# Performance work log

Hardware: AMD Instinct MI355X
Metric: run time of the kernel (lower is better)

The kernel has to match this reference:

```python
import jax, jax.numpy as jnp
import numpy as np

EMBED_DIM = 2048
NUM_Q_HEADS = 32
NUM_KV_HEADS = 8
HEAD_DIM = EMBED_DIM // NUM_Q_HEADS
N_REP = NUM_Q_HEADS // NUM_KV_HEADS
B, T = 2, 2048


def setup_inputs() -> dict:
    key = jax.random.key(0)
    ks = jax.random.split(key, 10)
    C = EMBED_DIM
    kv_dim = NUM_KV_HEADS * HEAD_DIM
    s = 1.0 / np.sqrt(C)
    return {
        "x": jax.random.normal(ks[0], (B, T, C), dtype=jnp.float32),
        "mask": jnp.tril(jnp.ones((1, 1, T, T), dtype=bool)),
        "Wq": jax.random.normal(ks[1], (C, C), dtype=jnp.float32) * s,
        "bq": jnp.zeros((C,), dtype=jnp.float32),
        "Wk": jax.random.normal(ks[2], (C, kv_dim), dtype=jnp.float32) * s,
        "bk": jnp.zeros((kv_dim,), dtype=jnp.float32),
        "Wv": jax.random.normal(ks[3], (C, kv_dim), dtype=jnp.float32) * s,
        "bv": jnp.zeros((kv_dim,), dtype=jnp.float32),
        "Wo": jax.random.normal(ks[4], (C, C), dtype=jnp.float32) * s,
        "bo": jnp.zeros((C,), dtype=jnp.float32),
    }


def reference(x, mask, Wq, bq, Wk, bk, Wv, bv, Wo, bo):
    b, t, c = x.shape
    # projections
    q = (x @ Wq + bq).reshape(b, t, NUM_Q_HEADS, HEAD_DIM).transpose(0, 2, 1, 3)   # [B,Hq,T,D]
    k = (x @ Wk + bk).reshape(b, t, NUM_KV_HEADS, HEAD_DIM).transpose(0, 2, 1, 3)  # [B,Hkv,T,D]
    v = (x @ Wv + bv).reshape(b, t, NUM_KV_HEADS, HEAD_DIM).transpose(0, 2, 1, 3)
    # repeat KV heads to match query heads (same math as expand+reshape)
    k = jnp.repeat(k, N_REP, axis=1)  # [B,Hq,T,D]
    v = jnp.repeat(v, N_REP, axis=1)
    scores = jnp.einsum("bhqd,bhkd->bhqk", q, k) / np.sqrt(HEAD_DIM)
    scores = jnp.where(mask, scores, -jnp.inf)
    attn = jax.nn.softmax(scores, axis=-1)
    out = jnp.einsum("bhqk,bhkd->bhqd", attn, v)  # [B,Hq,T,D]
    out = out.transpose(0, 2, 1, 3).reshape(b, t, c)
    return out @ Wo + bo
```

## Files before the change

kernel.cpp:

```cpp
#include <hip/hip_runtime.h>
#include <stdint.h>

typedef __attribute__((ext_vector_type(8))) short bf16x8;
typedef __attribute__((ext_vector_type(4))) float f32x4;

#define LOG2E 1.44269504088896f
#define T_SEQ 2048

__device__ __forceinline__ float bf2f(short s) {
    unsigned u = ((unsigned)(unsigned short)s) << 16;
    float f; __builtin_memcpy(&f, &u, 4); return f;
}
__device__ __forceinline__ short f2bf(float f) {
    unsigned u; __builtin_memcpy(&u, &f, 4);
    u = (u + 0x7FFFu + ((u >> 16) & 1u)) >> 16;
    return (short)u;
}
__device__ __forceinline__ short f2bf_trunc(float f) {
    unsigned u; __builtin_memcpy(&u, &f, 4);
    return (short)(u >> 16);
}

#define GLDS(g, l) __builtin_amdgcn_global_load_lds( \
    (const __attribute__((address_space(1))) void*)(g), \
    (__attribute__((address_space(3))) void*)(l), 16, 0, 0)

__global__ void detect_k(const unsigned short* __restrict__ x, int* __restrict__ flag) {
    int lane = threadIdx.x;
    int cnt = 0;
    for (int i = lane; i < 2048; i += 64) {
        int e = (x[i] >> 7) & 0xFF;
        if (e >= 0xC0) cnt++;
    }
    cnt += __shfl_xor(cnt, 1);
    cnt += __shfl_xor(cnt, 2);
    cnt += __shfl_xor(cnt, 4);
    cnt += __shfl_xor(cnt, 8);
    cnt += __shfl_xor(cnt, 16);
    cnt += __shfl_xor(cnt, 32);
    if (lane == 0) { flag[0] = (cnt >= 32) ? 1 : 0; flag[1] = 0; }
}

__global__ __launch_bounds__(256) void convert_k(
    const void* __restrict__ in, short* __restrict__ out, int n,
    const int* __restrict__ flag)
{
    int i = (blockIdx.x * 256 + threadIdx.x) * 8;
    if (i >= n) return;
    bf16x8 v;
    if (*flag) {
        const float* f = (const float*)in + i;
        #pragma unroll
        for (int j = 0; j < 8; ++j) v[j] = f2bf(f[j]);
    } else {
        v = *(const bf16x8*)((const short*)in + i);
    }
    *(bf16x8*)(out + i) = v;
}

__global__ __launch_bounds__(256) void convert4_k(
    const void* __restrict__ b0, const void* __restrict__ b1,
    const void* __restrict__ b2, const void* __restrict__ b3,
    short* __restrict__ o0, short* __restrict__ o1,
    short* __restrict__ o2, short* __restrict__ o3,
    const int* __restrict__ flag)
{
    int i = (blockIdx.x * 256 + threadIdx.x) * 8;
    const void* in; short* out; int off;
    if      (i < 2048) { in = b0; out = o0; off = i; }
    else if (i < 2560) { in = b1; out = o1; off = i - 2048; }
    else if (i < 3072) { in = b2; out = o2; off = i - 2560; }
    else if (i < 5120) { in = b3; out = o3; off = i - 3072; }
    else return;
    bf16x8 v;
    if (*flag) {
        const float* f = (const float*)in + off;
        #pragma unroll
        for (int j = 0; j < 8; ++j) v[j] = f2bf(f[j]);
    } else {
        v = *(const bf16x8*)((const short*)in + off);
    }
    *(bf16x8*)(out + off) = v;
}

__global__ __launch_bounds__(256) void transpose_k(
    const void* __restrict__ in_, short* __restrict__ out,
    int R, int ldi, long ibstride, long obstride, const int* __restrict__ flag)
{
    short* ob = out + (long)blockIdx.z * obstride;
    int c = blockIdx.x * 256 + threadIdx.x;
    int r0 = blockIdx.y * 64;
    int fp32 = *flag;
    if (fp32) {
        const float* ib = (const float*)in_ + (long)blockIdx.z * ibstride;
        for (int rr = 0; rr < 64; rr += 8) {
            bf16x8 v;
            #pragma unroll
            for (int j = 0; j < 8; ++j) v[j] = f2bf(ib[(long)(r0 + rr + j) * ldi + c]);
            *(bf16x8*)(ob + (long)c * R + r0 + rr) = v;
        }
    } else {
        const short* ib = (const short*)in_ + (long)blockIdx.z * ibstride;
        for (int rr = 0; rr < 64; rr += 8) {
            bf16x8 v;
            #pragma unroll
            for (int j = 0; j < 8; ++j) v[j] = ib[(long)(r0 + rr + j) * ldi + c];
            *(bf16x8*)(ob + (long)c * R + r0 + rr) = v;
        }
    }
}

#define BK 32
__global__ __launch_bounds__(256) void gemm_bt(
    const short* __restrict__ A, const short* __restrict__ Bt,
    const short* __restrict__ bias1, int nsplit,
    short* __restrict__ C, short* __restrict__ C2, int n2,
    float* __restrict__ Cf, const int* __restrict__ flag,
    int M, int N, int K)
{
    __shared__ short a_lds[128 * BK];
    __shared__ short b_lds[128 * BK];
    const int tid = threadIdx.x;
    const int wave = tid >> 6, lane = tid & 63;
    const int quad = lane >> 4, l16 = lane & 15;
    const int m0 = blockIdx.y * 128, n0 = blockIdx.x * 128;
    const int wm = (wave >> 1) * 64, wn = (wave & 1) * 64;

    const int c0 = wave * 64 + lane;
    const int c1 = 256 + c0;
    const int row0 = c0 >> 2, kc0 = (c0 & 3) ^ ((row0 >> 1) & 3);
    const int row1 = c1 >> 2, kc1 = (c1 & 3) ^ ((row1 >> 1) & 3);
    const long aoff0 = (long)(m0 + row0) * K + kc0 * 8;
    const long aoff1 = (long)(m0 + row1) * K + kc1 * 8;
    const long boff0 = (long)(n0 + row0) * K + kc0 * 8;
    const long boff1 = (long)(n0 + row1) * K + kc1 * 8;
    short* alp0 = a_lds + (wave * 64) * 8;
    short* alp1 = a_lds + (256 + wave * 64) * 8;
    short* blp0 = b_lds + (wave * 64) * 8;
    short* blp1 = b_lds + (256 + wave * 64) * 8;

    int aro[4], bro[4];
    #pragma unroll
    for (int t = 0; t < 4; ++t) {
        int ra = wm + t * 16 + l16;
        aro[t] = ra * BK + (quad ^ ((ra >> 1) & 3)) * 8;
        int rb = wn + t * 16 + l16;
        bro[t] = rb * BK + (quad ^ ((rb >> 1) & 3)) * 8;
    }

    f32x4 acc[4][4];
    #pragma unroll
    for (int i = 0; i < 4; ++i)
        #pragma unroll
        for (int j = 0; j < 4; ++j)
            acc[i][j] = (f32x4){0.f, 0.f, 0.f, 0.f};

    for (int k0 = 0; k0 < K; k0 += BK) {
        __syncthreads();
        GLDS(A + aoff0 + k0, alp0);
        GLDS(A + aoff1 + k0, alp1);
        GLDS(Bt + boff0 + k0, blp0);
        GLDS(Bt + boff1 + k0, blp1);
        __syncthreads();
        bf16x8 af[4], bfr[4];
        #pragma unroll
        for (int t = 0; t < 4; ++t) af[t] = *(const bf16x8*)(a_lds + aro[t]);
        #pragma unroll
        for (int t = 0; t < 4; ++t) bfr[t] = *(const bf16x8*)(b_lds + bro[t]);
        #pragma unroll
        for (int mt = 0; mt < 4; ++mt)
            #pragma unroll
            for (int nt = 0; nt < 4; ++nt)
                acc[mt][nt] = __builtin_amdgcn_mfma_f32_16x16x32_bf16(
                    af[mt], bfr[nt], acc[mt][nt], 0, 0, 0);
    }

    const int f32o = Cf ? *flag : 0;
    #pragma unroll
    for (int nt = 0; nt < 4; ++nt) {
        int col = n0 + wn + nt * 16 + l16;
        float bb = bf2f(bias1[col < nsplit ? col : 0]);
        #pragma unroll
        for (int mt = 0; mt < 4; ++mt)
            #pragma unroll
            for (int r = 0; r < 4; ++r) {
                int row = m0 + wm + mt * 16 + quad * 4 + r;
                float val = acc[mt][nt][r] + bb;
                if (f32o) {
                    Cf[(long)row * N + col] = val;
                } else if (C2) {
                    if (col < n2) C[(long)row * n2 + col] = f2bf(val);
                    else          C2[(long)row * (N - n2) + (col - n2)] = f2bf(val);
                } else {
                    C[(long)row * N + col] = f2bf(val);
                }
            }
    }
}

#define PLD 68
__global__ __launch_bounds__(256, 4) void attn_k(
    const short* __restrict__ Qf, const short* __restrict__ KVf,
    const short* __restrict__ Vt, short* __restrict__ Attn)
{
    __shared__ short k_lds[64 * PLD];
    __shared__ short vt_lds[64 * PLD];
    __shared__ short p_lds[4 * 32 * PLD];
    const int tid = threadIdx.x;
    const int wave = tid >> 6, lane = tid & 63;
    const int quad = lane >> 4, l16 = lane & 15;

    const int id = blockIdx.x;
    const int bh = id & 63;
    const int w = id >> 6;
    const int QTMAP[16] = {15,13,11,9, 0,2,4,6, 14,12,10,8, 1,3,5,7};
    const int qt = QTMAP[w];
    const int b = bh >> 5, h = bh & 31, hkv = h >> 2;
    const int q0 = qt * 128;
    const int nsteps = 2 * (qt + 1);

    bf16x8 aq[2][2];
    #pragma unroll
    for (int mt = 0; mt < 2; ++mt) {
        const short* qp = Qf + ((long)(b * T_SEQ + q0 + wave * 32 + mt * 16 + l16) * 2048
                                + h * 64 + quad * 8);
        aq[mt][0] = *(const bf16x8*)qp;
        aq[mt][1] = *(const bf16x8*)(qp + 32);
        #pragma unroll
        for (int j = 0; j < 8; ++j) {
            aq[mt][0][j] = f2bf(bf2f(aq[mt][0][j]) * 0.125f);
            aq[mt][1][j] = f2bf(bf2f(aq[mt][1][j]) * 0.125f);
        }
    }

    bf16x8 onesf;
    {
        short o = (l16 == 0) ? (short)0x3F80 : (short)0;
        #pragma unroll
        for (int j = 0; j < 8; ++j) onesf[j] = o;
    }

    f32x4 o_acc[2][4];
    f32x4 l_acc[2];
    #pragma unroll
    for (int mt = 0; mt < 2; ++mt) {
        l_acc[mt] = (f32x4){0.f, 0.f, 0.f, 0.f};
        #pragma unroll
        for (int dt = 0; dt < 4; ++dt) o_acc[mt][dt] = (f32x4){0.f, 0.f, 0.f, 0.f};
    }

    const int cA = tid, cB = 256 + tid;
    const int tA = cA >> 3, chA = cA & 7;
    const int tB = cB >> 3, chB = cB & 7;
    const short* kgA = KVf + ((long)(b * T_SEQ + tA) * 1024 + hkv * 64 + chA * 8);
    const short* kgB = KVf + ((long)(b * T_SEQ + tB) * 1024 + hkv * 64 + chB * 8);
    const short* vgA = Vt + ((long)((b * 8 + hkv) * 64 + tA) * 2048 + chA * 8);
    const short* vgB = Vt + ((long)((b * 8 + hkv) * 64 + tB) * 2048 + chB * 8);

    const int rowq0 = q0 + wave * 32 + quad * 4;
    short* pw = p_lds + (wave * 32 + quad * 4) * PLD + l16;
    const short* pr = p_lds + (wave * 32 + l16) * PLD + quad * 8;

    bf16x8 kA = *(const bf16x8*)(kgA);
    bf16x8 kB = *(const bf16x8*)(kgB);
    bf16x8 vA = *(const bf16x8*)(vgA);
    bf16x8 vB = *(const bf16x8*)(vgB);

    for (int s = 0; s < nsteps; ++s) {
        const int kt0 = s * 64;
        const int ktn = ((s + 1 < nsteps) ? (s + 1) : s) * 64;
        __syncthreads();
        *(bf16x8*)(k_lds + tA * PLD + chA * 8) = kA;
        *(bf16x8*)(k_lds + tB * PLD + chB * 8) = kB;
        *(bf16x8*)(vt_lds + tA * PLD + chA * 8) = vA;
        *(bf16x8*)(vt_lds + tB * PLD + chB * 8) = vB;
        kA = *(const bf16x8*)(kgA + (long)ktn * 1024);
        kB = *(const bf16x8*)(kgB + (long)ktn * 1024);
        vA = *(const bf16x8*)(vgA + ktn);
        vB = *(const bf16x8*)(vgB + ktn);
        __syncthreads();

        const int masked = (kt0 >= q0);
        #pragma unroll
        for (int nt = 0; nt < 4; ++nt) {
            bf16x8 bk0 = *(const bf16x8*)(k_lds + (nt * 16 + l16) * PLD + quad * 8);
            bf16x8 bk1 = *(const bf16x8*)(k_lds + (nt * 16 + l16) * PLD + 32 + quad * 8);
            #pragma unroll
            for (int mt = 0; mt < 2; ++mt) {
                f32x4 z = (f32x4){0.f, 0.f, 0.f, 0.f};
                z = __builtin_amdgcn_mfma_f32_16x16x32_bf16(aq[mt][0], bk0, z, 0, 0, 0);
                z = __builtin_amdgcn_mfma_f32_16x16x32_bf16(aq[mt][1], bk1, z, 0, 0, 0);
                if (!masked) {
                    #pragma unroll
                    for (int r = 0; r < 4; ++r)
                        z[r] = exp2f(fmaf(z[r], LOG2E, -16.0f));
                } else {
                    const int rowq = rowq0 + mt * 16;
                    const int tcol = kt0 + nt * 16 + l16;
                    #pragma unroll
                    for (int r = 0; r < 4; ++r) {
                        float e = exp2f(fmaf(z[r], LOG2E, -16.0f));
                        z[r] = (tcol <= rowq + r) ? e : 0.0f;
                    }
                }
                #pragma unroll
                for (int r = 0; r < 4; ++r)
                    pw[mt * 16 * PLD + r * PLD + nt * 16] = f2bf_trunc(z[r]);
            }
        }

        bf16x8 ap[2][2];
        #pragma unroll
        for (int mt = 0; mt < 2; ++mt) {
            ap[mt][0] = *(const bf16x8*)(pr + mt * 16 * PLD);
            ap[mt][1] = *(const bf16x8*)(pr + mt * 16 * PLD + 32);
        }
        #pragma unroll
        for (int dt = 0; dt < 4; ++dt) {
            bf16x8 bv0 = *(const bf16x8*)(vt_lds + (dt * 16 + l16) * PLD + quad * 8);
            bf16x8 bv1 = *(const bf16x8*)(vt_lds + (dt * 16 + l16) * PLD + 32 + quad * 8);
            #pragma unroll
            for (int mt = 0; mt < 2; ++mt) {
                o_acc[mt][dt] = __builtin_amdgcn_mfma_f32_16x16x32_bf16(ap[mt][0], bv0, o_acc[mt][dt], 0, 0, 0);
                o_acc[mt][dt] = __builtin_amdgcn_mfma_f32_16x16x32_bf16(ap[mt][1], bv1, o_acc[mt][dt], 0, 0, 0);
            }
        }
        #pragma unroll
        for (int mt = 0; mt < 2; ++mt) {
            l_acc[mt] = __builtin_amdgcn_mfma_f32_16x16x32_bf16(ap[mt][0], onesf, l_acc[mt], 0, 0, 0);
            l_acc[mt] = __builtin_amdgcn_mfma_f32_16x16x32_bf16(ap[mt][1], onesf, l_acc[mt], 0, 0, 0);
        }
    }

    #pragma unroll
    for (int mt = 0; mt < 2; ++mt)
        #pragma unroll
        for (int r = 0; r < 4; ++r) {
            const float linv = 1.0f / __shfl(l_acc[mt][r], quad << 4);
            const int rowo = q0 + wave * 32 + mt * 16 + quad * 4 + r;
            short* ap = Attn + (long)(b * T_SEQ + rowo) * 2048 + h * 64 + l16;
            #pragma unroll
            for (int dt = 0; dt < 4; ++dt)
                ap[dt * 16] = f2bf(o_acc[mt][dt][r] * linv);
        }
}

extern "C" void kernel_launch(void* const* d_in, const int* in_sizes, int n_in,
                              void* d_out, int out_size, void* d_ws, size_t ws_size,
                              hipStream_t stream) {
    const void* x  = d_in[0];
    const void* Wq = d_in[2];
    const void* bq = d_in[3];
    const void* Wk = d_in[4];
    const void* bk = d_in[5];
    const void* Wv = d_in[6];
    const void* bv = d_in[7];
    const void* Wo = d_in[8];
    const void* bo = d_in[9];

    short* ws    = (short*)d_ws;
    int*   flags = (int*)ws;
    short* base  = ws + 16;
    short* xb    = base;
    short* Wq_t  = xb + (long)8388608;
    short* Wkv_t = Wq_t + (long)4194304;
    short* regB  = base + (long)17039360;
    short* bqb   = regB;
    short* bkb   = bqb + 2048;
    short* bvb   = bkb + 512;
    short* bob   = bvb + 512;
    short* Wo_t  = bob + 2048;
    short* Qf    = Wo_t + (long)4194304;
    short* KVf   = Qf + (long)8388608;
    short* Vtp   = KVf + (long)4194304;
    short* Attn  = Vtp + (long)2097152;

    detect_k<<<1, 64, 0, stream>>>((const unsigned short*)x, flags);

    convert_k<<<4096, 256, 0, stream>>>(x, xb, 4096 * 2048, flags);
    convert4_k<<<3, 256, 0, stream>>>(bq, bk, bv, bo, bqb, bkb, bvb, bob, flags);

    transpose_k<<<dim3(8, 32, 1), 256, 0, stream>>>(Wq, Wq_t, 2048, 2048, 0L, 0L, flags);
    transpose_k<<<dim3(2, 32, 1), 256, 0, stream>>>(Wk, Wkv_t, 2048, 512, 0L, 0L, flags);
    transpose_k<<<dim3(2, 32, 1), 256, 0, stream>>>(Wv, Wkv_t + (long)512 * 2048, 2048, 512, 0L, 0L, flags);
    transpose_k<<<dim3(8, 32, 1), 256, 0, stream>>>(Wo, Wo_t, 2048, 2048, 0L, 0L, flags);

    gemm_bt<<<dim3(24, 32), 256, 0, stream>>>(xb, Wq_t, bqb, 3072,
                                              Qf, KVf, 2048, nullptr, flags,
                                              4096, 3072, 2048);

    transpose_k<<<dim3(2, 32, 2), 256, 0, stream>>>(KVf + 512, Vtp, 2048, 1024,
                                                    (long)2048 * 1024, (long)512 * 2048, flags + 1);

    attn_k<<<1024, 256, 0, stream>>>(Qf, KVf, Vtp, Attn);

    gemm_bt<<<dim3(16, 32), 256, 0, stream>>>(Attn, Wo_t, bob, 2048,
                                              (short*)d_out, nullptr, 0,
                                              (float*)d_out, flags,
                                              4096, 2048, 2048);
}
```

Baseline: 457.8 us.

## Replace GEMM with 256-row double-buffered LDS kernel using 512 threads

Replaces the 128x128 single-buffered GEMM with a templated 256xBN tile kernel of 8 waves that double-buffers LDS. The next K-slice is prefetched via global_load_lds while MFMAs run on the current one, with explicit vmcnt waits and s_setprio around the MFMA bursts. The larger tile raises operand reuse per LDS load and halves the number of barriers per tile. In exchange it uses more registers and LDS per block, and the grids shrink to 192 and 256 blocks, which may leave CUs underused.

```diff
diff --git a/kernel.cpp b/kernel.cpp
--- a/kernel.cpp
+++ b/kernel.cpp
@@ -24,6 +24,12 @@
 #define GLDS(g, l) __builtin_amdgcn_global_load_lds( \
     (const __attribute__((address_space(1))) void*)(g), \
     (__attribute__((address_space(3))) void*)(l), 16, 0, 0)
+
+__device__ __forceinline__ void fence_barrier() {
+    asm volatile("" ::: "memory");
+    __builtin_amdgcn_s_barrier();
+    asm volatile("" ::: "memory");
+}
 
 __global__ void detect_k(const unsigned short* __restrict__ x, int* __restrict__ flag) {
     int lane = threadIdx.x;
@@ -110,78 +116,106 @@
     }
 }
 
-#define BK 32
-__global__ __launch_bounds__(256) void gemm_bt(
+template <int BN>
+__global__ __launch_bounds__(512, 1) void gemm256_k(
     const short* __restrict__ A, const short* __restrict__ Bt,
     const short* __restrict__ bias1, int nsplit,
     short* __restrict__ C, short* __restrict__ C2, int n2,
     float* __restrict__ Cf, const int* __restrict__ flag,
     int M, int N, int K)
 {
-    __shared__ short a_lds[128 * BK];
-    __shared__ short b_lds[128 * BK];
+    constexpr int NT = BN / 64;
+    __shared__ short a_lds[2][256 * 32];
+    __shared__ short b_lds[2][BN * 32];
     const int tid = threadIdx.x;
     const int wave = tid >> 6, lane = tid & 63;
     const int quad = lane >> 4, l16 = lane & 15;
-    const int m0 = blockIdx.y * 128, n0 = blockIdx.x * 128;
-    const int wm = (wave >> 1) * 64, wn = (wave & 1) * 64;
-
-    const int c0 = wave * 64 + lane;
-    const int c1 = 256 + c0;
-    const int row0 = c0 >> 2, kc0 = (c0 & 3) ^ ((row0 >> 1) & 3);
-    const int row1 = c1 >> 2, kc1 = (c1 & 3) ^ ((row1 >> 1) & 3);
-    const long aoff0 = (long)(m0 + row0) * K + kc0 * 8;
-    const long aoff1 = (long)(m0 + row1) * K + kc1 * 8;
-    const long boff0 = (long)(n0 + row0) * K + kc0 * 8;
-    const long boff1 = (long)(n0 + row1) * K + kc1 * 8;
-    short* alp0 = a_lds + (wave * 64) * 8;
-    short* alp1 = a_lds + (256 + wave * 64) * 8;
-    short* blp0 = b_lds + (wave * 64) * 8;
-    short* blp1 = b_lds + (256 + wave * 64) * 8;
-
-    int aro[4], bro[4];
-    #pragma unroll
-    for (int t = 0; t < 4; ++t) {
-        int ra = wm + t * 16 + l16;
-        aro[t] = ra * BK + (quad ^ ((ra >> 1) & 3)) * 8;
-        int rb = wn + t * 16 + l16;
-        bro[t] = rb * BK + (quad ^ ((rb >> 1) & 3)) * 8;
-    }
-
-    f32x4 acc[4][4];
-    #pragma unroll
-    for (int i = 0; i < 4; ++i)
-        #pragma unroll
-        for (int j = 0; j < 4; ++j)
+    const int m0 = blockIdx.y * 256, n0 = blockIdx.x * BN;
+    const int wm = (wave >> 2) * 128;
+    const int wn = (wave & 3) * (BN / 4);
+
+    const int rA0 = tid >> 2,         kA0 = (tid & 3) ^ ((rA0 >> 1) & 3);
+    const int rA1 = (512 + tid) >> 2, kA1 = (tid & 3) ^ ((rA1 >> 1) & 3);
+    const long aoff0 = (long)(m0 + rA0) * K + kA0 * 8;
+    const long aoff1 = (long)(m0 + rA1) * K + kA1 * 8;
+    const long boff0 = (long)(n0 + rA0) * K + kA0 * 8;
+    const long boff1 = (long)(n0 + rA1) * K + kA1 * 8;
+
+    int aro[8], bro[NT];
+    #pragma unroll
+    for (int mt = 0; mt < 8; ++mt) {
+        int ra = wm + mt * 16 + l16;
+        aro[mt] = ra * 32 + (quad ^ ((ra >> 1) & 3)) * 8;
+    }
+    #pragma unroll
+    for (int nt = 0; nt < NT; ++nt) {
+        int rb = wn + nt * 16 + l16;
+        bro[nt] = rb * 32 + (quad ^ ((rb >> 1) & 3)) * 8;
+    }
+
+    f32x4 acc[8][NT];
+    #pragma unroll
+    for (int i = 0; i < 8; ++i)
+        #pragma unroll
+        for (int j = 0; j < NT; ++j)
             acc[i][j] = (f32x4){0.f, 0.f, 0.f, 0.f};
 
-    for (int k0 = 0; k0 < K; k0 += BK) {
-        __syncthreads();
-        GLDS(A + aoff0 + k0, alp0);
-        GLDS(A + aoff1 + k0, alp1);
-        GLDS(Bt + boff0 + k0, blp0);
-        GLDS(Bt + boff1 + k0, blp1);
-        __syncthreads();
-        bf16x8 af[4], bfr[4];
-        #pragma unroll
-        for (int t = 0; t < 4; ++t) af[t] = *(const bf16x8*)(a_lds + aro[t]);
-        #pragma unroll
-        for (int t = 0; t < 4; ++t) bfr[t] = *(const bf16x8*)(b_lds + bro[t]);
+    const int nk = K >> 5;
+    GLDS(A + aoff0, &a_lds[0][0] + wave * 512);
+    GLDS(A + aoff1, &a_lds[0][0] + 4096 + wave * 512);
+    GLDS(Bt + boff0, &b_lds[0][0] + wave * 512);
+    if constexpr (BN == 256) GLDS(Bt + boff1, &b_lds[0][0] + 4096 + wave * 512);
+
+    for (int t = 0; t < nk; ++t) {
+        const int p = t & 1;
+        const long kn = (long)((t + 1 < nk) ? t + 1 : t) * 32;
+        short* an = &a_lds[p ^ 1][0];
+        short* bn = &b_lds[p ^ 1][0];
+        GLDS(A + aoff0 + kn, an + wave * 512);
+        GLDS(A + aoff1 + kn, an + 4096 + wave * 512);
+        GLDS(Bt + boff0 + kn, bn + wave * 512);
+        if constexpr (BN == 256) GLDS(Bt + boff1 + kn, bn + 4096 + wave * 512);
+
+        if constexpr (BN == 256) asm volatile("s_waitcnt vmcnt(4)" ::: "memory");
+        else                     asm volatile("s_waitcnt vmcnt(3)" ::: "memory");
+        fence_barrier();
+
+        const short* ac = &a_lds[p][0];
+        const short* bc = &b_lds[p][0];
+        bf16x8 bfr[NT], af[4];
+        #pragma unroll
+        for (int nt = 0; nt < NT; ++nt) bfr[nt] = *(const bf16x8*)(bc + bro[nt]);
+        #pragma unroll
+        for (int mt = 0; mt < 4; ++mt) af[mt] = *(const bf16x8*)(ac + aro[mt]);
+        __builtin_amdgcn_s_setprio(1);
         #pragma unroll
         for (int mt = 0; mt < 4; ++mt)
             #pragma unroll
-            for (int nt = 0; nt < 4; ++nt)
+            for (int nt = 0; nt < NT; ++nt)
                 acc[mt][nt] = __builtin_amdgcn_mfma_f32_16x16x32_bf16(
                     af[mt], bfr[nt], acc[mt][nt], 0, 0, 0);
+        __builtin_amdgcn_s_setprio(0);
+        #pragma unroll
+        for (int mt = 0; mt < 4; ++mt) af[mt] = *(const bf16x8*)(ac + aro[mt + 4]);
+        __builtin_amdgcn_s_setprio(1);
+        #pragma unroll
+        for (int mt = 0; mt < 4; ++mt)
+            #pragma unroll
+            for (int nt = 0; nt < NT; ++nt)
+                acc[mt + 4][nt] = __builtin_amdgcn_mfma_f32_16x16x32_bf16(
+                    af[mt], bfr[nt], acc[mt + 4][nt], 0, 0, 0);
+        __builtin_amdgcn_s_setprio(0);
+        asm volatile("s_waitcnt lgkmcnt(0)" ::: "memory");
+        fence_barrier();
     }
 
     const int f32o = Cf ? *flag : 0;
     #pragma unroll
-    for (int nt = 0; nt < 4; ++nt) {
+    for (int nt = 0; nt < NT; ++nt) {
         int col = n0 + wn + nt * 16 + l16;
         float bb = bf2f(bias1[col < nsplit ? col : 0]);
         #pragma unroll
-        for (int mt = 0; mt < 4; ++mt)
+        for (int mt = 0; mt < 8; ++mt)
             #pragma unroll
             for (int r = 0; r < 4; ++r) {
                 int row = m0 + wm + mt * 16 + quad * 4 + r;
@@ -385,17 +419,17 @@
     transpose_k<<<dim3(2, 32, 1), 256, 0, stream>>>(Wv, Wkv_t + (long)512 * 2048, 2048, 512, 0L, 0L, flags);
     transpose_k<<<dim3(8, 32, 1), 256, 0, stream>>>(Wo, Wo_t, 2048, 2048, 0L, 0L, flags);
 
-    gemm_bt<<<dim3(24, 32), 256, 0, stream>>>(xb, Wq_t, bqb, 3072,
-                                              Qf, KVf, 2048, nullptr, flags,
-                                              4096, 3072, 2048);
+    gemm256_k<256><<<dim3(12, 16), 512, 0, stream>>>(xb, Wq_t, bqb, 3072,
+                                                     Qf, KVf, 2048, nullptr, flags,
+                                                     4096, 3072, 2048);
 
     transpose_k<<<dim3(2, 32, 2), 256, 0, stream>>>(KVf + 512, Vtp, 2048, 1024,
                                                     (long)2048 * 1024, (long)512 * 2048, flags + 1);
 
     attn_k<<<1024, 256, 0, stream>>>(Qf, KVf, Vtp, Attn);
 
-    gemm_bt<<<dim3(16, 32), 256, 0, stream>>>(Attn, Wo_t, bob, 2048,
-                                              (short*)d_out, nullptr, 0,
-                                              (float*)d_out, flags,
-                                              4096, 2048, 2048);
-}
+    gemm256_k<128><<<dim3(16, 16), 512, 0, stream>>>(Attn, Wo_t, bob, 2048,
+                                                     (short*)d_out, nullptr, 0,
+                                                     (float*)d_out, flags,
+                                                     4096, 2048, 2048);
+}
```

Result: slower. 469.2 us (+2.5%).
